# Optimization experiments

Measured on AMD Instinct MI355X. Metric: run time of the kernel, lower is better.

The kernel has to match this reference:

```python
import jax, jax.numpy as jnp
import numpy as np
from jax import lax

B, T, C_IN, H, K = 8, 4096, 256, 256, 3


def _conv1d_same(x_nct, w_oik, b_o):
    # x: [B, C, T], w: [H, C, K], b: [H] -> [B, H, T], 'same' padding
    y = lax.conv_general_dilated(x_nct, w_oik, window_strides=(1,),
                                 padding='SAME',
                                 dimension_numbers=('NCH', 'OIH', 'NCH'))
    return y + b_o[None, :, None]


def setup_inputs() -> dict:
    key = jax.random.key(0)
    ks = jax.random.split(key, 7)
    std = 1.0 / np.sqrt(H)
    u = lambda k, shape: jax.random.uniform(k, shape, jnp.float32, -std, std)
    return {
        'inputs': jax.random.normal(ks[0], (B, T, C_IN), jnp.float32),
        'init_f': jax.random.normal(ks[1], (B, H), jnp.float32),
        'init_z': jax.random.normal(ks[2], (B, H), jnp.float32),
        'f_w': u(ks[3], (H, C_IN, K)),
        'f_b': u(ks[4], (H,)),
        'z_w': u(ks[5], (H, C_IN, K)),
        'z_b': u(ks[6], (H,)),
    }


def reference(inputs, init_f, init_z, f_w, f_b, z_w, z_b):
    x = jnp.transpose(inputs, (0, 2, 1))                    # [B, C, T]
    raw_f = jnp.transpose(_conv1d_same(x, f_w, f_b), (0, 2, 1))  # [B, T, H]
    raw_z = jnp.transpose(_conv1d_same(x, z_w, z_b), (0, 2, 1))
    # prepend init state along time: init_state[0] -> f, init_state[1] -> z
    raw_f = jnp.concatenate([init_f[:, None, :], raw_f], axis=1)  # [B, T+1, H]
    raw_z = jnp.concatenate([init_z[:, None, :], raw_z], axis=1)
    log_one_minus_f = jax.nn.log_sigmoid(-raw_f)
    log_z = jax.nn.log_sigmoid(raw_z)
    log_f = jax.nn.log_sigmoid(raw_f)
    cs = jnp.cumsum(log_f, axis=1)
    recurrent_gates = log_f - cs + cs[:, -1:, :]
    log_hidden = lax.cumlogsumexp(log_z + log_one_minus_f + recurrent_gates, axis=1)
    return jnp.exp(log_hidden - recurrent_gates)            # [B, T+1, H]
```

## Files before the change

kernel.cpp:

```cpp
#include <hip/hip_runtime.h>
#include <hip/hip_bf16.h>

#define B_ 8
#define T_ 4096
#define C_ 256
#define H_ 256
#define K_ 3
#define NC 128
#define TC 32
#define WFRAG_ELEMS (24 * 32 * 64 * 8)

typedef __attribute__((ext_vector_type(8))) __bf16 bf16x8;
typedef __attribute__((ext_vector_type(4))) float f32x4;

__device__ __forceinline__ float sigm(float x) { return 1.0f / (1.0f + __expf(-x)); }

__device__ __forceinline__ ushort f2bf(float f) {
    union { float f; unsigned u; } v; v.f = f;
    return (ushort)((v.u + 0x7FFFu + ((v.u >> 16) & 1u)) >> 16);
}
__device__ __forceinline__ float bf2f(ushort u) {
    union { unsigned u; float f; } v; v.u = ((unsigned)u) << 16; return v.f;
}

__global__ __launch_bounds__(256) void wfrag_kernel(const float* __restrict__ fw,
                                                    const float* __restrict__ zw,
                                                    ushort* __restrict__ wfrag) {
    int idx = blockIdx.x * 256 + threadIdx.x;
    if (idx >= WFRAG_ELEMS) return;
    int j   = idx & 7;
    int l   = (idx >> 3) & 63;
    int ntg = (idx >> 9) & 31;
    int ks  = idx >> 14;
    int n = ntg * 16 + (l & 15);
    int kappa = ks * 32 + (l >> 4) * 8 + j;
    int k = kappa >> 8, c = kappa & 255;
    const float* w = (n < 256) ? fw : zw;
    int h = n & 255;
    wfrag[idx] = f2bf(w[(h * C_ + c) * K_ + k]);
}

__device__ __forceinline__ void bload(const ushort* wb, int ks, const int (&ntg)[4],
                                      bf16x8 (&dst)[4]) {
#pragma unroll
    for (int ni = 0; ni < 4; ++ni)
        dst[ni] = *(const bf16x8*)(wb + (size_t)ks * 16384 + (size_t)ntg[ni] * 512);
}

__device__ __forceinline__ void conv_step(const char* smem, int ks, int lr, int lg,
                                          const bf16x8 (&bfr)[4], f32x4 (&acc)[4][4]) {
    const int k = ks >> 3;
    const int cb = ((ks & 7) * 32 + lg * 8) * 2;
    bf16x8 afr[4];
#pragma unroll
    for (int mi = 0; mi < 4; ++mi) {
        int row = mi * 16 + lr + k;
        afr[mi] = *(const bf16x8*)(smem + row * 512 + (cb ^ ((row & 7) << 4)));
    }
#pragma unroll
    for (int ni = 0; ni < 4; ++ni)
#pragma unroll
        for (int mi = 0; mi < 4; ++mi)
            acc[mi][ni] = __builtin_amdgcn_mfma_f32_16x16x32_bf16(afr[mi], bfr[ni], acc[mi][ni], 0, 0, 0);
}

template <int P>
__device__ __forceinline__ void epi_write(f32x4 (&acc)[4][4], unsigned* buf,
                                          int lr, int lg, int h0) {
#pragma unroll
    for (int m2 = 0; m2 < 2; ++m2) {
        const int mi = 2 * P + m2;
#pragma unroll
        for (int ni = 0; ni < 2; ++ni) {
            const int h = h0 + ni * 16 + lr;
#pragma unroll
            for (int r = 0; r < 4; ++r) {
                float fv = sigm(acc[mi][ni][r]);
                float av = sigm(acc[mi][ni + 2][r]) * (1.0f - fv);
                int tl = m2 * 16 + lg * 4 + r;
                buf[tl * 256 + (h ^ ((tl << 2) & 31))] =
                    (unsigned)f2bf(av) | ((unsigned)f2bf(fv) << 16);
            }
        }
    }
}

template <int P>
__device__ __forceinline__ void chunk_scan(const unsigned* buf, int b, int bx, int tid,
                                           unsigned* AP, unsigned* APl, float* fl) {
    if (tid < 256) {
        const int h = tid;
        const int chunk = bx * 2 + P;
        const int r0 = chunk * TC;
        unsigned* app = AP + ((size_t)b * T_ + r0) * H_ + h;
        unsigned u = buf[h];
        float A = bf2f((ushort)(u & 0xffff));
        float Pp = 1.0f;
        float f_prev = bf2f((ushort)(u >> 16));
        unsigned upk = (unsigned)f2bf(A) | ((unsigned)f2bf(Pp) << 16);
        app[0] = upk;
#pragma unroll 8
        for (int j = 1; j < TC; ++j) {
            u = buf[j * 256 + (h ^ ((j << 2) & 31))];
            float a = bf2f((ushort)(u & 0xffff));
            float f = bf2f((ushort)(u >> 16));
            A = fmaf(f_prev, A, a);
            Pp *= f_prev;
            f_prev = f;
            upk = (unsigned)f2bf(A) | ((unsigned)f2bf(Pp) << 16);
            app[(size_t)j * H_] = upk;
        }
        APl[((size_t)b * NC + chunk) * H_ + h] = upk;
        fl[((size_t)b * NC + chunk) * H_ + h] = f_prev;
    }
}

__global__ __launch_bounds__(512, 4) void conv_scan_kernel(const float* __restrict__ x,
                                                           const ushort* __restrict__ wfrag,
                                                           const float* __restrict__ fb,
                                                           const float* __restrict__ zb,
                                                           unsigned* __restrict__ AP,
                                                           unsigned* __restrict__ APl,
                                                           float* __restrict__ fl) {
    __shared__ __align__(16) char smem[66 * 512];
    unsigned* buf = (unsigned*)smem;

    const int b = blockIdx.y;
    const int t0 = blockIdx.x * 64;
    const int tid = threadIdx.x;

    for (int idx = tid; idx < 66 * 64; idx += 512) {
        int row = idx >> 6;
        int c4 = (idx & 63) * 4;
        int t = t0 - 1 + row;
        float4 v = make_float4(0.f, 0.f, 0.f, 0.f);
        if (t >= 0 && t < T_) v = *(const float4*)(x + ((size_t)(b * T_ + t)) * C_ + c4);
        ushort4 w4;
        w4.x = f2bf(v.x); w4.y = f2bf(v.y); w4.z = f2bf(v.z); w4.w = f2bf(v.w);
        *(ushort4*)(smem + row * 512 + ((c4 * 2) ^ ((row & 7) << 4))) = w4;
    }
    __syncthreads();

    const int wv = tid >> 6;
    const int l  = tid & 63;
    const int lr = l & 15;
    const int lg = l >> 4;
    const int h0 = wv * 32;

    f32x4 acc[4][4];
#pragma unroll
    for (int ni = 0; ni < 4; ++ni) {
        float bv = (ni < 2 ? fb : zb)[h0 + (ni & 1) * 16 + lr];
        f32x4 bvv = {bv, bv, bv, bv};
#pragma unroll
        for (int mi = 0; mi < 4; ++mi) acc[mi][ni] = bvv;
    }

    const ushort* wb = wfrag + (size_t)l * 8;
    int ntg_[4];
#pragma unroll
    for (int ni = 0; ni < 4; ++ni)
        ntg_[ni] = (ni < 2) ? (wv * 2 + ni) : (16 + wv * 2 + ni - 2);

    bf16x8 ba[4], bb[4];
    bload(wb, 0, ntg_, ba);
#pragma unroll 1
    for (int ks = 0; ks < 24; ks += 2) {
        bload(wb, ks + 1, ntg_, bb);
        conv_step(smem, ks, lr, lg, ba, acc);
        if (ks + 2 < 24) bload(wb, ks + 2, ntg_, ba);
        conv_step(smem, ks + 1, lr, lg, bb, acc);
    }

    __syncthreads();
    epi_write<0>(acc, buf, lr, lg, h0);
    __syncthreads();
    chunk_scan<0>(buf, b, blockIdx.x, tid, AP, APl, fl);

    __syncthreads();
    epi_write<1>(acc, buf, lr, lg, h0);
    __syncthreads();
    chunk_scan<1>(buf, b, blockIdx.x, tid, AP, APl, fl);
}

__global__ __launch_bounds__(256) void combine_kernel(const unsigned* __restrict__ APl,
                                                      const float* __restrict__ fl,
                                                      const float* __restrict__ init_f,
                                                      const float* __restrict__ init_z,
                                                      float* __restrict__ out,
                                                      float* __restrict__ sin_) {
    const int b = blockIdx.x;
    const int h = threadIdx.x;
    float f0 = sigm(init_f[b * H_ + h]);
    float z0 = sigm(init_z[b * H_ + h]);
    float s = z0 * (1.0f - f0);
    out[(size_t)b * (T_ + 1) * H_ + h] = s;
    float flp = f0;
    const unsigned* ap = APl + (size_t)b * NC * H_ + h;
    const float* fp = fl + (size_t)b * NC * H_ + h;
    float* sp = sin_ + (size_t)b * NC * H_ + h;
#pragma unroll 8
    for (int c = 0; c < NC; ++c) {
        unsigned u = ap[(size_t)c * H_];
        float fln = fp[(size_t)c * H_];
        float st = flp * s;
        sp[(size_t)c * H_] = st;
        s = fmaf(bf2f((ushort)(u >> 16)), st, bf2f((ushort)(u & 0xffff)));
        flp = fln;
    }
}

__global__ __launch_bounds__(256) void apply_kernel(const unsigned* __restrict__ AP,
                                                    const float* __restrict__ sin_,
                                                    float* __restrict__ out) {
    const int c = blockIdx.x;
    const int b = blockIdx.y;
    const int tid = threadIdx.x;
    const int jr = tid >> 6;
    const int h4 = (tid & 63) * 4;
    const int r0 = c * TC;
    const float4 s4 = *(const float4*)(sin_ + ((size_t)b * NC + c) * H_ + h4);
#pragma unroll
    for (int p = 0; p < 8; ++p) {
        const int j = p * 4 + jr;
        const uint4 u4 = *(const uint4*)(AP + ((size_t)b * T_ + r0 + j) * H_ + h4);
        float4 o;
        o.x = fmaf(bf2f((ushort)(u4.x >> 16)), s4.x, bf2f((ushort)(u4.x & 0xffff)));
        o.y = fmaf(bf2f((ushort)(u4.y >> 16)), s4.y, bf2f((ushort)(u4.y & 0xffff)));
        o.z = fmaf(bf2f((ushort)(u4.z >> 16)), s4.z, bf2f((ushort)(u4.z & 0xffff)));
        o.w = fmaf(bf2f((ushort)(u4.w >> 16)), s4.w, bf2f((ushort)(u4.w & 0xffff)));
        *(float4*)(out + ((size_t)b * (T_ + 1) + r0 + 1 + j) * H_ + h4) = o;
    }
}

extern "C" void kernel_launch(void* const* d_in, const int* in_sizes, int n_in,
                              void* d_out, int out_size, void* d_ws, size_t ws_size,
                              hipStream_t stream) {
    const float* inputs = (const float*)d_in[0];
    const float* init_f = (const float*)d_in[1];
    const float* init_z = (const float*)d_in[2];
    const float* f_w    = (const float*)d_in[3];
    const float* f_b    = (const float*)d_in[4];
    const float* z_w    = (const float*)d_in[5];
    const float* z_b    = (const float*)d_in[6];
    float* out = (float*)d_out;

    ushort* wfrag = (ushort*)d_ws;
    unsigned* AP  = (unsigned*)(wfrag + WFRAG_ELEMS);
    unsigned* APl = AP + (size_t)B_ * T_ * H_;
    float* fl     = (float*)(APl + (size_t)B_ * NC * H_);
    float* sin_   = fl + (size_t)B_ * NC * H_;

    wfrag_kernel<<<(WFRAG_ELEMS + 255) / 256, 256, 0, stream>>>(f_w, z_w, wfrag);

    dim3 cgrid(T_ / 64, B_, 1);
    conv_scan_kernel<<<cgrid, 512, 0, stream>>>(inputs, wfrag, f_b, z_b, AP, APl, fl);

    combine_kernel<<<B_, H_, 0, stream>>>(APl, fl, init_f, init_z, out, sin_);

    dim3 agrid(NC, B_, 1);
    apply_kernel<<<agrid, 256, 0, stream>>>(AP, sin_, out);
}
```

Baseline: 68.84 us.

## Scan both time chunks concurrently with all threads and use packed bf16 convert

The epilogue now writes both 32-row chunks into a larger 64KB shared buffer at once, so all 512 threads run the two chunk scans in parallel instead of half the threads scanning each chunk in turn with extra barriers. Float-to-bf16 packing uses the hardware v_cvt_pk_bf16_f32 instruction instead of manual rounding, and interior blocks skip the boundary checks when loading x. The larger shared allocation may lower how many blocks fit per CU.

```diff
diff --git a/kernel.cpp b/kernel.cpp
--- a/kernel.cpp
+++ b/kernel.cpp
@@ -21,6 +21,11 @@
 }
 __device__ __forceinline__ float bf2f(ushort u) {
     union { unsigned u; float f; } v; v.u = ((unsigned)u) << 16; return v.f;
+}
+__device__ __forceinline__ unsigned cvt_pk_bf16(float lo, float hi) {
+    unsigned r;
+    asm("v_cvt_pk_bf16_f32 %0, %1, %2" : "=v"(r) : "v"(lo), "v"(hi));
+    return r;
 }
 
 __global__ __launch_bounds__(256) void wfrag_kernel(const float* __restrict__ fw,
@@ -64,57 +69,6 @@
             acc[mi][ni] = __builtin_amdgcn_mfma_f32_16x16x32_bf16(afr[mi], bfr[ni], acc[mi][ni], 0, 0, 0);
 }
 
-template <int P>
-__device__ __forceinline__ void epi_write(f32x4 (&acc)[4][4], unsigned* buf,
-                                          int lr, int lg, int h0) {
-#pragma unroll
-    for (int m2 = 0; m2 < 2; ++m2) {
-        const int mi = 2 * P + m2;
-#pragma unroll
-        for (int ni = 0; ni < 2; ++ni) {
-            const int h = h0 + ni * 16 + lr;
-#pragma unroll
-            for (int r = 0; r < 4; ++r) {
-                float fv = sigm(acc[mi][ni][r]);
-                float av = sigm(acc[mi][ni + 2][r]) * (1.0f - fv);
-                int tl = m2 * 16 + lg * 4 + r;
-                buf[tl * 256 + (h ^ ((tl << 2) & 31))] =
-                    (unsigned)f2bf(av) | ((unsigned)f2bf(fv) << 16);
-            }
-        }
-    }
-}
-
-template <int P>
-__device__ __forceinline__ void chunk_scan(const unsigned* buf, int b, int bx, int tid,
-                                           unsigned* AP, unsigned* APl, float* fl) {
-    if (tid < 256) {
-        const int h = tid;
-        const int chunk = bx * 2 + P;
-        const int r0 = chunk * TC;
-        unsigned* app = AP + ((size_t)b * T_ + r0) * H_ + h;
-        unsigned u = buf[h];
-        float A = bf2f((ushort)(u & 0xffff));
-        float Pp = 1.0f;
-        float f_prev = bf2f((ushort)(u >> 16));
-        unsigned upk = (unsigned)f2bf(A) | ((unsigned)f2bf(Pp) << 16);
-        app[0] = upk;
-#pragma unroll 8
-        for (int j = 1; j < TC; ++j) {
-            u = buf[j * 256 + (h ^ ((j << 2) & 31))];
-            float a = bf2f((ushort)(u & 0xffff));
-            float f = bf2f((ushort)(u >> 16));
-            A = fmaf(f_prev, A, a);
-            Pp *= f_prev;
-            f_prev = f;
-            upk = (unsigned)f2bf(A) | ((unsigned)f2bf(Pp) << 16);
-            app[(size_t)j * H_] = upk;
-        }
-        APl[((size_t)b * NC + chunk) * H_ + h] = upk;
-        fl[((size_t)b * NC + chunk) * H_ + h] = f_prev;
-    }
-}
-
 __global__ __launch_bounds__(512, 4) void conv_scan_kernel(const float* __restrict__ x,
                                                            const ushort* __restrict__ wfrag,
                                                            const float* __restrict__ fb,
@@ -122,22 +76,32 @@
                                                            unsigned* __restrict__ AP,
                                                            unsigned* __restrict__ APl,
                                                            float* __restrict__ fl) {
-    __shared__ __align__(16) char smem[66 * 512];
+    __shared__ __align__(16) char smem[65536];
     unsigned* buf = (unsigned*)smem;
 
     const int b = blockIdx.y;
     const int t0 = blockIdx.x * 64;
     const int tid = threadIdx.x;
 
-    for (int idx = tid; idx < 66 * 64; idx += 512) {
-        int row = idx >> 6;
-        int c4 = (idx & 63) * 4;
-        int t = t0 - 1 + row;
-        float4 v = make_float4(0.f, 0.f, 0.f, 0.f);
-        if (t >= 0 && t < T_) v = *(const float4*)(x + ((size_t)(b * T_ + t)) * C_ + c4);
-        ushort4 w4;
-        w4.x = f2bf(v.x); w4.y = f2bf(v.y); w4.z = f2bf(v.z); w4.w = f2bf(v.w);
-        *(ushort4*)(smem + row * 512 + ((c4 * 2) ^ ((row & 7) << 4))) = w4;
+    if (blockIdx.x == 0 || blockIdx.x == gridDim.x - 1) {
+        for (int idx = tid; idx < 66 * 64; idx += 512) {
+            int row = idx >> 6;
+            int c4 = (idx & 63) * 4;
+            int t = t0 - 1 + row;
+            float4 v = make_float4(0.f, 0.f, 0.f, 0.f);
+            if (t >= 0 && t < T_) v = *(const float4*)(x + ((size_t)(b * T_ + t)) * C_ + c4);
+            uint2 w2 = make_uint2(cvt_pk_bf16(v.x, v.y), cvt_pk_bf16(v.z, v.w));
+            *(uint2*)(smem + row * 512 + ((c4 * 2) ^ ((row & 7) << 4))) = w2;
+        }
+    } else {
+        for (int idx = tid; idx < 66 * 64; idx += 512) {
+            int row = idx >> 6;
+            int c4 = (idx & 63) * 4;
+            int t = t0 - 1 + row;
+            float4 v = *(const float4*)(x + ((size_t)(b * T_ + t)) * C_ + c4);
+            uint2 w2 = make_uint2(cvt_pk_bf16(v.x, v.y), cvt_pk_bf16(v.z, v.w));
+            *(uint2*)(smem + row * 512 + ((c4 * 2) ^ ((row & 7) << 4))) = w2;
+        }
     }
     __syncthreads();
 
@@ -173,14 +137,50 @@
     }
 
     __syncthreads();
-    epi_write<0>(acc, buf, lr, lg, h0);
+#pragma unroll
+    for (int mi = 0; mi < 4; ++mi) {
+#pragma unroll
+        for (int ni = 0; ni < 2; ++ni) {
+            const int h = h0 + ni * 16 + lr;
+#pragma unroll
+            for (int r = 0; r < 4; ++r) {
+                float fv = sigm(acc[mi][ni][r]);
+                float av = sigm(acc[mi][ni + 2][r]) * (1.0f - fv);
+                int tl = (mi & 1) * 16 + lg * 4 + r;
+                int trow = (mi >> 1) * 32 + tl;
+                buf[trow * 256 + (h ^ ((tl << 2) & 31))] = cvt_pk_bf16(av, fv);
+            }
+        }
+    }
     __syncthreads();
-    chunk_scan<0>(buf, b, blockIdx.x, tid, AP, APl, fl);
-
-    __syncthreads();
-    epi_write<1>(acc, buf, lr, lg, h0);
-    __syncthreads();
-    chunk_scan<1>(buf, b, blockIdx.x, tid, AP, APl, fl);
+
+    {
+        const int ch = tid >> 8;
+        const int h = tid & 255;
+        const int chunk = blockIdx.x * 2 + ch;
+        const int r0 = chunk * TC;
+        const unsigned* bp = buf + ch * 32 * 256;
+        unsigned* app = AP + ((size_t)b * T_ + r0) * H_ + h;
+        unsigned u = bp[h];
+        float A = bf2f((ushort)(u & 0xffff));
+        float Pp = 1.0f;
+        float f_prev = bf2f((ushort)(u >> 16));
+        unsigned upk = cvt_pk_bf16(A, Pp);
+        app[0] = upk;
+#pragma unroll 8
+        for (int j = 1; j < TC; ++j) {
+            u = bp[j * 256 + (h ^ ((j << 2) & 31))];
+            float a = bf2f((ushort)(u & 0xffff));
+            float f = bf2f((ushort)(u >> 16));
+            A = fmaf(f_prev, A, a);
+            Pp *= f_prev;
+            f_prev = f;
+            upk = cvt_pk_bf16(A, Pp);
+            app[(size_t)j * H_] = upk;
+        }
+        APl[((size_t)b * NC + chunk) * H_ + h] = upk;
+        fl[((size_t)b * NC + chunk) * H_ + h] = f_prev;
+    }
 }
 
 __global__ __launch_bounds__(256) void combine_kernel(const unsigned* __restrict__ APl,
```

After: 66.19 us. 1.04x faster.
